# Kernel optimization log

Hardware: AMD Instinct MI355X
Metric: run time of the kernel (lower is better)

## Reference

```python
import jax, jax.numpy as jnp
import numpy as np

H = 128   # hidden_dim
E = 768   # embedding_dim
L = 20    # num_layers
B = 64    # batch
T = 512   # seq_len


def setup_inputs() -> dict:
    key = jax.random.key(0)
    ks = jax.random.split(key, 9)
    k = 1.0 / np.sqrt(H)  # PyTorch LSTM default init scale
    u = lambda kk, shape: jax.random.uniform(kk, shape, jnp.float32, -k, k)
    return {
        "x": jax.random.normal(ks[0], (B, T, E), jnp.float32),
        "Wih0": u(ks[1], (4 * H, E)),        # layer 0 input weights
        "Whh0": u(ks[2], (4 * H, H)),
        "bih0": u(ks[3], (4 * H,)),
        "bhh0": u(ks[4], (4 * H,)),
        "Wih": u(ks[5], (L - 1, 4 * H, H)),  # layers 1..19
        "Whh": u(ks[6], (L - 1, 4 * H, H)),
        "bih": u(ks[7], (L - 1, 4 * H)),
        "bhh": u(ks[8], (L - 1, 4 * H)),
    }


def _lstm_layer(xs, Wih, Whh, b):
    # xs: [T, B, Din] -> ys: [T, B, H], h_final: [B, H]
    bsz = xs.shape[1]
    pre = jnp.einsum('tbd,gd->tbg', xs, Wih) + b  # precompute input projections

    def step(carry, pt):
        h, c = carry
        g = pt + h @ Whh.T  # [B, 4H]
        i, f, gg, o = jnp.split(g, 4, axis=-1)  # PyTorch gate order i,f,g,o
        i = jax.nn.sigmoid(i)
        f = jax.nn.sigmoid(f)
        gg = jnp.tanh(gg)
        o = jax.nn.sigmoid(o)
        c = f * c + i * gg
        h = o * jnp.tanh(c)
        return (h, c), h

    init = (jnp.zeros((bsz, H), xs.dtype), jnp.zeros((bsz, H), xs.dtype))
    (_, _), ys = jax.lax.scan(step, init, pre)
    return ys, ys[-1]


def reference(x, Wih0, Whh0, bih0, bhh0, Wih, Whh, bih, bhh):
    xs = jnp.swapaxes(x, 0, 1)  # [T, B, E]
    ys, _ = _lstm_layer(xs, Wih0, Whh0, bih0 + bhh0)

    def layer_fn(ys, params):
        Wl, Wh, bi, bh = params
        ys2, h = _lstm_layer(ys, Wl, Wh, bi + bh)
        return ys2, h

    ys, hs = jax.lax.scan(layer_fn, ys, (Wih, Whh, bih, bhh))
    return hs[-1]  # hidden state of last (20th) layer at final timestep: [B, H]
```

## Files before the change

### kernel.cpp

```cpp
#include <hip/hip_runtime.h>

#define H4 128
#define EE 768
#define NL 20
#define BB 64
#define TT 512
#define G4 512
#define NBG 8
#define CK 16
#define NCH (TT/CK)
#define RC 2

typedef _Float16 v8h __attribute__((ext_vector_type(8)));
typedef _Float16 v4h __attribute__((ext_vector_type(4)));
typedef float v4f __attribute__((ext_vector_type(4)));
typedef unsigned int v4u __attribute__((ext_vector_type(4)));

#if defined(__has_builtin)
#if __has_builtin(__builtin_amdgcn_exp2f) && __has_builtin(__builtin_amdgcn_rcpf)
#define EXP2F __builtin_amdgcn_exp2f
#define RCPF  __builtin_amdgcn_rcpf
#endif
#endif
#ifndef EXP2F
#define EXP2F exp2f
#define RCPF(x) (1.0f/(x))
#endif

__device__ __forceinline__ float fast_sig(float x) {
  float e = EXP2F(-1.44269504f * x);
  return RCPF(1.0f + e);
}
__device__ __forceinline__ float fast_tanh(float x) {
  float e = EXP2F(2.88539008f * x);
  return 1.0f - 2.0f * RCPF(1.0f + e);
}

__device__ __forceinline__ int swz(int row, int byteInRow) {
  return (row * 256 + byteInRow) ^ ((row & 7) << 4);
}

__global__ __launch_bounds__(256) void prep_kernel(
    const float* __restrict__ Wih0, const float* __restrict__ Whh0,
    const float* __restrict__ bih,  const float* __restrict__ bhh,
    const float* __restrict__ Wih,  const float* __restrict__ Whh,
    _Float16* __restrict__ W0h, _Float16* __restrict__ Wc,
    float* __restrict__ biasc, unsigned* __restrict__ flags)
{
  long idx = (long)blockIdx.x * 256 + threadIdx.x;
  const long NWC = (long)NL * G4 * 256;
  const long NW0 = (long)G4 * EE;
  const long NBI = (long)NL * G4;
  if (idx < NWC) {
    int l = (int)(idx >> 17);
    int rem = (int)(idx & 131071);
    int n = rem >> 8, kk = rem & 255;
    float v;
    if (l == 0) v = (kk < 128) ? 0.0f : Whh0[n * H4 + kk - 128];
    else v = (kk < 128) ? Wih[((long)(l-1) * G4 + n) * H4 + kk]
                        : Whh[((long)(l-1) * G4 + n) * H4 + kk - 128];
    Wc[idx] = (_Float16)v;
  } else if ((idx -= NWC) < NW0) {
    W0h[idx] = (_Float16)Wih0[idx];
  } else if ((idx -= NW0) < NBI) {
    int l = (int)(idx >> 9), n = (int)(idx & 511);
    biasc[idx] = (l == 0) ? 0.0f : (bih[(l-1) * G4 + n] + bhh[(l-1) * G4 + n]);
  } else if ((idx -= NBI) < 256) {
    flags[idx] = 0u;
  }
}

__global__ __launch_bounds__(512) void pre0_gemm(
    const float* __restrict__ x, const _Float16* __restrict__ W0h,
    const float* __restrict__ bih0, const float* __restrict__ bhh0,
    _Float16* __restrict__ pre0)
{
  __shared__ __align__(16) unsigned char smem[46080];
  _Float16* sA = (_Float16*)smem;
  _Float16* sB = (_Float16*)(smem + 5120);
  _Float16* sC = (_Float16*)smem;
  int t = blockIdx.x;
  int tid = threadIdx.x;
  int w = tid >> 6, lane = tid & 63;
  int l15 = lane & 15, kb = lane >> 4;

  v4f acc[4][4];
#pragma unroll
  for (int mi = 0; mi < 4; ++mi)
#pragma unroll
    for (int ni = 0; ni < 4; ++ni) acc[mi][ni] = (v4f){0.f, 0.f, 0.f, 0.f};

  int bA = tid >> 3, kqA = tid & 7;
  const float* xp = x + ((long)bA * TT + t) * EE + kqA * 4;
  const _Float16* wp = W0h + (long)tid * EE;

  for (int k0 = 0; k0 < EE; k0 += 32) {
    float4 xv = *(const float4*)(xp + k0);
    v4h xh = { (_Float16)xv.x, (_Float16)xv.y, (_Float16)xv.z, (_Float16)xv.w };
    *(v4h*)&sA[bA * 40 + kqA * 4] = xh;
#pragma unroll
    for (int c = 0; c < 4; ++c)
      *(v8h*)&sB[tid * 40 + c * 8] = *(const v8h*)(wp + k0 + c * 8);
    __syncthreads();
#pragma unroll
    for (int mi = 0; mi < 4; ++mi) {
      v8h a = *(const v8h*)&sA[(16 * mi + l15) * 40 + kb * 8];
#pragma unroll
      for (int ni = 0; ni < 4; ++ni) {
        v8h b = *(const v8h*)&sB[(64 * w + 16 * ni + l15) * 40 + kb * 8];
        acc[mi][ni] = __builtin_amdgcn_mfma_f32_16x16x32_f16(a, b, acc[mi][ni], 0, 0, 0);
      }
    }
    __syncthreads();
  }

#pragma unroll
  for (int hh2 = 0; hh2 < 2; ++hh2) {
    __syncthreads();
    if ((w >> 2) == hh2) {
      int wl = w & 3;
#pragma unroll
      for (int ni = 0; ni < 4; ++ni) {
        int nloc = 64 * wl + 16 * ni + l15;
        int n = 256 * hh2 + nloc;
        float bia = bih0[n] + bhh0[n];
#pragma unroll
        for (int mi = 0; mi < 4; ++mi)
#pragma unroll
          for (int r = 0; r < 4; ++r)
            sC[nloc * 72 + 16 * mi + 4 * kb + r] = (_Float16)(acc[mi][ni][r] + bia);
      }
    }
    __syncthreads();
    int row = tid >> 1, part = tid & 1;
    int n = 256 * hh2 + row;
#pragma unroll
    for (int g = 0; g < 4; ++g) {
      int bg = part * 4 + g;
      _Float16* po = pre0 + (((long)t * 8 + bg) * 512 + n) * 8;
      *(v8h*)po = *(const v8h*)&sC[row * 72 + part * 32 + g * 8];
    }
  }
}

__global__ __launch_bounds__(512, 1) void lstm_pipe(
    const _Float16* __restrict__ pre0, const _Float16* __restrict__ Wc,
    const float* __restrict__ biasc, _Float16* __restrict__ yring,
    unsigned* __restrict__ flags, float* __restrict__ out)
{
  __shared__ __align__(16) unsigned char lds[40960];
  const int l = blockIdx.x >> 3, bg = blockIdx.x & 7;
  const int tid = threadIdx.x, w = tid >> 6, lane = tid & 63;
  const int l15 = lane & 15, kb = lane >> 4;
  const int jloc = 16 * w + l15;
  const bool valid = (kb < 2);
  const int b0 = 4 * (kb & 1);

  v8h bw[4][8];
  const _Float16* wbase = Wc + (long)l * G4 * 256;
#pragma unroll
  for (int q = 0; q < 4; ++q)
#pragma unroll
    for (int ks = 0; ks < 8; ++ks)
      bw[q][ks] = *(const v8h*)(wbase + (long)(128 * q + jloc) * 256 + ks * 32 + kb * 8);

  float bias_q[4];
#pragma unroll
  for (int q = 0; q < 4; ++q)
    bias_q[q] = (l == 0) ? 0.0f : biasc[l * G4 + 128 * q + jloc];

  *(v4u*)(lds + 32768 + tid * 16) = (v4u){0u, 0u, 0u, 0u};

  const int myf = l * 8 + bg;
  const unsigned* fin  = flags + ((l > 0) ? (myf - 8) : myf);
  const unsigned* fout = flags + ((l < NL - 1) ? (myf + 8) : myf);
  unsigned* fme = flags + myf;
  char* ywr = (char*)(yring + (long)myf * (RC * CK * 1024));
  const char* yrd = (const char*)(yring + (long)(myf - 8) * (RC * CK * 1024));

  v4f cst = (v4f){0.f, 0.f, 0.f, 0.f};
  v4h pc[4];
  const _Float16* pbase0 = pre0 + (long)bg * 4096 + jloc * 8 + b0;
  if (l == 0) {
#pragma unroll
    for (int q = 0; q < 4; ++q)
      pc[q] = *(const v4h*)(pbase0 + q * 1024);
  }

  __syncthreads();

  for (int c = 0; c < NCH; ++c) {
    if (l > 0) {
      unsigned f;
      for (;;) {
        asm volatile("global_load_dword %0, %1, off sc0 sc1\n\ts_waitcnt vmcnt(0)"
                     : "=v"(f) : "v"(fin));
        if (f > (unsigned)c) break;
        __builtin_amdgcn_s_sleep(2);
      }
      const char* src = yrd + (long)(c & (RC - 1)) * 32768 + tid * 16;
      v4u d0, d1, d2, d3;
      asm volatile("global_load_dwordx4 %0, %1, off sc0 sc1" : "=v"(d0) : "v"(src));
      asm volatile("global_load_dwordx4 %0, %1, off sc0 sc1" : "=v"(d1) : "v"(src + 8192));
      asm volatile("global_load_dwordx4 %0, %1, off sc0 sc1" : "=v"(d2) : "v"(src + 16384));
      asm volatile("global_load_dwordx4 %0, %1, off sc0 sc1" : "=v"(d3) : "v"(src + 24576));
      asm volatile("s_waitcnt vmcnt(0)" ::: "memory");
      __builtin_amdgcn_sched_barrier(0);
      unsigned char* dst = lds + tid * 16;
      *(v4u*)(dst)         = d0;
      *(v4u*)(dst +  8192) = d1;
      *(v4u*)(dst + 16384) = d2;
      *(v4u*)(dst + 24576) = d3;
    }
    if (l < NL - 1 && c >= RC) {
      unsigned f;
      for (;;) {
        asm volatile("global_load_dword %0, %1, off sc0 sc1\n\ts_waitcnt vmcnt(0)"
                     : "=v"(f) : "v"(fout));
        if (f >= (unsigned)(c - 1)) break;
        __builtin_amdgcn_s_sleep(2);
      }
    }
    __syncthreads();

    for (int ts = 0; ts < CK; ++ts) {
      const int t = c * CK + ts;
      const int p = t & 1;
      v4f acc[4];
#pragma unroll
      for (int q = 0; q < 4; ++q)
        acc[q] = (v4f){bias_q[q], bias_q[q], bias_q[q], bias_q[q]};

      v4h pn[4];
      if (l == 0) {
#pragma unroll
        for (int q = 0; q < 4; ++q)
#pragma unroll
          for (int r = 0; r < 4; ++r) acc[q][r] += (float)pc[q][r];
        const int tn = (t + 1) & (TT - 1);
        const _Float16* pb = pbase0 + (long)tn * 32768;
#pragma unroll
        for (int q = 0; q < 4; ++q)
          pn[q] = *(const v4h*)(pb + q * 1024);
      }

      const unsigned char* hb = lds + 32768 + p * 4096;
      if (l > 0) {
        const unsigned char* yb = lds + ts * 2048;
#pragma unroll
        for (int ks = 0; ks < 4; ++ks) {
          v8h a = *(const v8h*)(yb + swz(l15, ks * 64 + kb * 16));
#pragma unroll
          for (int q = 0; q < 4; ++q)
            acc[q] = __builtin_amdgcn_mfma_f32_16x16x32_f16(a, bw[q][ks], acc[q], 0, 0, 0);
        }
      }
#pragma unroll
      for (int ks = 4; ks < 8; ++ks) {
        v8h a = *(const v8h*)(hb + swz(l15, (ks - 4) * 64 + kb * 16));
#pragma unroll
        for (int q = 0; q < 4; ++q)
          acc[q] = __builtin_amdgcn_mfma_f32_16x16x32_f16(a, bw[q][ks], acc[q], 0, 0, 0);
      }

      _Float16 hh[4]; float hf[4];
#pragma unroll
      for (int r = 0; r < 4; ++r) {
        float i_ = fast_sig(acc[0][r]);
        float f_ = fast_sig(acc[1][r]);
        float g_ = fast_tanh(acc[2][r]);
        float o_ = fast_sig(acc[3][r]);
        float cn = f_ * cst[r] + i_ * g_;
        cst[r] = cn;
        float h_ = o_ * fast_tanh(cn);
        hf[r] = h_; hh[r] = (_Float16)h_;
      }

      if (valid) {
        unsigned char* hn = lds + 32768 + (p ^ 1) * 4096;
#pragma unroll
        for (int r = 0; r < 4; ++r)
          *(_Float16*)(hn + swz(b0 + r, jloc * 2)) = hh[r];
        if (l == NL - 1 && t == TT - 1) {
#pragma unroll
          for (int r = 0; r < 4; ++r)
            out[(bg * 8 + b0 + r) * H4 + jloc] = hf[r];
        }
      }
      if (l == 0) {
#pragma unroll
        for (int q = 0; q < 4; ++q) pc[q] = pn[q];
      }
      __syncthreads();

      if (l < NL - 1) {
        unsigned hv = *(const unsigned*)(lds + 32768 + (p ^ 1) * 4096 + tid * 4);
        char* dst = ywr + (long)(c & (RC - 1)) * 32768 + ts * 2048 + tid * 4;
        asm volatile("global_store_dword %0, %1, off sc0 sc1"
                     :: "v"(dst), "v"(hv) : "memory");
      }
    }

    asm volatile("s_waitcnt vmcnt(0)" ::: "memory");
    __syncthreads();
    if (tid == 0) {
      unsigned v = (unsigned)(c + 1);
      asm volatile("global_store_dword %0, %1, off sc0 sc1" :: "v"(fme), "v"(v) : "memory");
    }
  }
}

extern "C" void kernel_launch(void* const* d_in, const int* in_sizes, int n_in,
                              void* d_out, int out_size, void* d_ws, size_t ws_size,
                              hipStream_t stream)
{
  const float* x    = (const float*)d_in[0];
  const float* Wih0 = (const float*)d_in[1];
  const float* Whh0 = (const float*)d_in[2];
  const float* bih0 = (const float*)d_in[3];
  const float* bhh0 = (const float*)d_in[4];
  const float* Wih  = (const float*)d_in[5];
  const float* Whh  = (const float*)d_in[6];
  const float* bih  = (const float*)d_in[7];
  const float* bhh  = (const float*)d_in[8];
  float* out = (float*)d_out;
  char* ws = (char*)d_ws;

  _Float16* pre0  = (_Float16*)(ws);
  _Float16* W0h   = (_Float16*)(ws + 33554432);
  _Float16* Wc    = (_Float16*)(ws + 34340864);
  float*    bc    = (float*)   (ws + 39583744);
  _Float16* yring = (_Float16*)(ws + 39624704);
  unsigned* flags = (unsigned*)(ws + 50110464);

  prep_kernel<<<11817, 256, 0, stream>>>(Wih0, Whh0, bih, bhh, Wih, Whh, W0h, Wc, bc, flags);
  pre0_gemm<<<TT, 512, 0, stream>>>(x, W0h, bih0, bhh0, pre0);
  lstm_pipe<<<NL * NBG, 512, 0, stream>>>(pre0, Wc, bc, yring, flags, out);
}
```

Measured before the change: 1.101 ms.

## Stage layer-0 input projections per chunk into LDS and use raw barriers

Layer 0 blocks now load a whole 16-timestep chunk of precomputed input projections (128KB) into LDS at the start of each chunk, instead of prefetching one step's values into registers from global memory every timestep. LDS grows to 136KB to hold them. The __syncthreads calls are replaced with an explicit lgkmcnt wait plus s_barrier and sched_barrier, and the memory clobber is dropped from the y-ring store. The aim is to take per-step global-load latency off layer 0's critical recurrent path and to cut barrier overhead. The cost is a large burst load per chunk that is not overlapped with compute, plus the risk of weaker memory ordering.

Result: faster. 1.072 ms (-2.6%).

```diff
diff --git a/kernel.cpp b/kernel.cpp
--- a/kernel.cpp
+++ b/kernel.cpp
@@ -10,6 +10,7 @@
 #define CK 16
 #define NCH (TT/CK)
 #define RC 2
+#define HB 131072
 
 typedef _Float16 v8h __attribute__((ext_vector_type(8)));
 typedef _Float16 v4h __attribute__((ext_vector_type(4)));
@@ -148,7 +149,7 @@
     const float* __restrict__ biasc, _Float16* __restrict__ yring,
     unsigned* __restrict__ flags, float* __restrict__ out)
 {
-  __shared__ __align__(16) unsigned char lds[40960];
+  __shared__ __align__(16) unsigned char lds[HB + 8192];
   const int l = blockIdx.x >> 3, bg = blockIdx.x & 7;
   const int tid = threadIdx.x, w = tid >> 6, lane = tid & 63;
   const int l15 = lane & 15, kb = lane >> 4;
@@ -169,7 +170,7 @@
   for (int q = 0; q < 4; ++q)
     bias_q[q] = (l == 0) ? 0.0f : biasc[l * G4 + 128 * q + jloc];
 
-  *(v4u*)(lds + 32768 + tid * 16) = (v4u){0u, 0u, 0u, 0u};
+  *(v4u*)(lds + HB + tid * 16) = (v4u){0u, 0u, 0u, 0u};
 
   const int myf = l * 8 + bg;
   const unsigned* fin  = flags + ((l > 0) ? (myf - 8) : myf);
@@ -177,15 +178,9 @@
   unsigned* fme = flags + myf;
   char* ywr = (char*)(yring + (long)myf * (RC * CK * 1024));
   const char* yrd = (const char*)(yring + (long)(myf - 8) * (RC * CK * 1024));
+  const char* pre0b = (const char*)pre0;
 
   v4f cst = (v4f){0.f, 0.f, 0.f, 0.f};
-  v4h pc[4];
-  const _Float16* pbase0 = pre0 + (long)bg * 4096 + jloc * 8 + b0;
-  if (l == 0) {
-#pragma unroll
-    for (int q = 0; q < 4; ++q)
-      pc[q] = *(const v4h*)(pbase0 + q * 1024);
-  }
 
   __syncthreads();
 
@@ -211,6 +206,16 @@
       *(v4u*)(dst +  8192) = d1;
       *(v4u*)(dst + 16384) = d2;
       *(v4u*)(dst + 24576) = d3;
+    } else {
+      v4u d[16];
+#pragma unroll
+      for (int ts = 0; ts < CK; ++ts) {
+        const char* s = pre0b + ((long)(c * CK + ts) * 8 + bg) * 8192 + tid * 16;
+        d[ts] = *(const v4u*)s;
+      }
+#pragma unroll
+      for (int ts = 0; ts < CK; ++ts)
+        *(v4u*)(lds + ts * 8192 + tid * 16) = d[ts];
     }
     if (l < NL - 1 && c >= RC) {
       unsigned f;
@@ -221,7 +226,9 @@
         __builtin_amdgcn_s_sleep(2);
       }
     }
-    __syncthreads();
+    asm volatile("s_waitcnt lgkmcnt(0)" ::: "memory");
+    __builtin_amdgcn_s_barrier();
+    __builtin_amdgcn_sched_barrier(0);
 
     for (int ts = 0; ts < CK; ++ts) {
       const int t = c * CK + ts;
@@ -231,21 +238,16 @@
       for (int q = 0; q < 4; ++q)
         acc[q] = (v4f){bias_q[q], bias_q[q], bias_q[q], bias_q[q]};
 
-      v4h pn[4];
+      const unsigned char* hb = lds + HB + p * 4096;
       if (l == 0) {
-#pragma unroll
-        for (int q = 0; q < 4; ++q)
-#pragma unroll
-          for (int r = 0; r < 4; ++r) acc[q][r] += (float)pc[q][r];
-        const int tn = (t + 1) & (TT - 1);
-        const _Float16* pb = pbase0 + (long)tn * 32768;
-#pragma unroll
-        for (int q = 0; q < 4; ++q)
-          pn[q] = *(const v4h*)(pb + q * 1024);
-      }
-
-      const unsigned char* hb = lds + 32768 + p * 4096;
-      if (l > 0) {
+        const unsigned char* pbts = lds + ts * 8192 + (kb & 1) * 8;
+#pragma unroll
+        for (int q = 0; q < 4; ++q) {
+          v4h pv = *(const v4h*)(pbts + (128 * q + jloc) * 16);
+#pragma unroll
+          for (int r = 0; r < 4; ++r) acc[q][r] += (float)pv[r];
+        }
+      } else {
         const unsigned char* yb = lds + ts * 2048;
 #pragma unroll
         for (int ks = 0; ks < 4; ++ks) {
@@ -277,7 +279,7 @@
       }
 
       if (valid) {
-        unsigned char* hn = lds + 32768 + (p ^ 1) * 4096;
+        unsigned char* hn = lds + HB + (p ^ 1) * 4096;
 #pragma unroll
         for (int r = 0; r < 4; ++r)
           *(_Float16*)(hn + swz(b0 + r, jloc * 2)) = hh[r];
@@ -287,22 +289,21 @@
             out[(bg * 8 + b0 + r) * H4 + jloc] = hf[r];
         }
       }
-      if (l == 0) {
-#pragma unroll
-        for (int q = 0; q < 4; ++q) pc[q] = pn[q];
-      }
-      __syncthreads();
+
+      asm volatile("s_waitcnt lgkmcnt(0)" ::: "memory");
+      __builtin_amdgcn_s_barrier();
+      __builtin_amdgcn_sched_barrier(0);
 
       if (l < NL - 1) {
-        unsigned hv = *(const unsigned*)(lds + 32768 + (p ^ 1) * 4096 + tid * 4);
+        unsigned hv = *(const unsigned*)(lds + HB + (p ^ 1) * 4096 + tid * 4);
         char* dst = ywr + (long)(c & (RC - 1)) * 32768 + ts * 2048 + tid * 4;
-        asm volatile("global_store_dword %0, %1, off sc0 sc1"
-                     :: "v"(dst), "v"(hv) : "memory");
+        asm volatile("global_store_dword %0, %1, off sc0 sc1" :: "v"(dst), "v"(hv));
       }
     }
 
     asm volatile("s_waitcnt vmcnt(0)" ::: "memory");
-    __syncthreads();
+    __builtin_amdgcn_s_barrier();
+    __builtin_amdgcn_sched_barrier(0);
     if (tid == 0) {
       unsigned v = (unsigned)(c + 1);
       asm volatile("global_store_dword %0, %1, off sc0 sc1" :: "v"(fme), "v"(v) : "memory");
```
